# Optimization experiments

Hardware: AMD Instinct MI355X
Metric: run time of the kernel (lower is better)

## Reference

```python
import jax, jax.numpy as jnp
import numpy as np

PATCH = (4, 4, 4)
EMBED_DIM = 768
MASK_RATIO = 0.75
LN_EPS = 1e-3  # keras LayerNormalization default epsilon


def _sin_pos_enc_3d(nH, nW, nD, embed_dim):
    # Mirrors SinPosEncoding3D: per-axis sin/cos interleaved, concat, truncate.
    channels = int(np.ceil(embed_dim / 6) * 2)
    if channels % 2:
        channels += 1
    inv_freq = jnp.asarray(
        1.0 / np.power(10000, np.arange(0, channels, 2) / np.float32(channels)),
        dtype=jnp.float32)

    def emb1(n):
        s = jnp.arange(n, dtype=jnp.float32)[:, None] * inv_freq[None, :]  # [n, channels//2]
        return jnp.stack([jnp.sin(s), jnp.cos(s)], axis=-1).reshape(n, channels)

    ex = jnp.broadcast_to(emb1(nH)[:, None, None, :], (nH, nW, nD, channels))
    ey = jnp.broadcast_to(emb1(nW)[None, :, None, :], (nH, nW, nD, channels))
    ez = jnp.broadcast_to(emb1(nD)[None, None, :, :], (nH, nW, nD, channels))
    emb = jnp.concatenate([ex, ey, ez], axis=-1)[..., :embed_dim]
    return emb.reshape(1, nH * nW * nD, embed_dim)  # [1, token_num, E]


def setup_inputs() -> dict:
    key = jax.random.key(0)
    k1, k2, k3, k4 = jax.random.split(key, 4)
    B, H, W, D, C = 4, 96, 96, 96, 1
    nH, nW, nD = H // PATCH[0], W // PATCH[1], D // PATCH[2]
    token_num = nH * nW * nD
    mask_num = int(token_num * MASK_RATIO)
    patch_dim = PATCH[0] * PATCH[1] * PATCH[2] * C
    return {
        "x": jax.random.normal(k1, (B, H, W, D, C), dtype=jnp.float32),
        "proj_w": jax.random.normal(k2, (patch_dim, EMBED_DIM), dtype=jnp.float32) * 0.02,
        "proj_b": jnp.zeros((EMBED_DIM,), dtype=jnp.float32),
        "mask_token": jax.random.normal(k3, (1, mask_num, patch_dim), dtype=jnp.float32),
        "gamma": jnp.ones((EMBED_DIM,), dtype=jnp.float32),
        "beta": jnp.zeros((EMBED_DIM,), dtype=jnp.float32),
        "perm": jax.random.permutation(k4, token_num).astype(jnp.int32),
    }


def reference(x, proj_w, proj_b, mask_token, gamma, beta, perm):
    B, H, W, D, C = x.shape
    p0, p1, p2 = PATCH
    nH, nW, nD = H // p0, W // p1, D // p2
    token_num = nH * nW * nD
    mask_num = int(token_num * MASK_RATIO)

    # im2col-style 3D patch extraction (matches tf.extract_volume_patches layout)
    patches = x.reshape(B, nH, p0, nW, p1, nD, p2, C)
    patches = patches.transpose(0, 1, 3, 5, 2, 4, 6, 7)
    patches_flat = patches.reshape(B, token_num, p0 * p1 * p2 * C)

    mask_idx = perm[:mask_num]
    unmask_idx = perm[mask_num:]

    penc = _sin_pos_enc_3d(nH, nW, nD, EMBED_DIM)  # [1, token_num, E]

    # unmasked tokens: gather -> dense proj -> pos-enc add
    unmask_tokens = jnp.take(patches_flat, unmask_idx, axis=1)       # [B, U, pdim]
    a = jnp.einsum('bup,pe->bue', unmask_tokens, proj_w) + proj_b \
        + jnp.take(penc, unmask_idx, axis=1)                          # [B, U, E]

    # masked tokens: learned mask token -> proj -> pos-enc add, broadcast over B
    b = jnp.einsum('omp,pe->ome', mask_token, proj_w) + proj_b \
        + jnp.take(penc, mask_idx, axis=1)                            # [1, M, E]
    b = jnp.broadcast_to(b, (B, mask_num, EMBED_DIM))

    out = jnp.concatenate([a, b], axis=1).reshape(B, nH, nW, nD, EMBED_DIM)

    # LayerNorm over last axis (keras default: eps=1e-3)
    mean = jnp.mean(out, axis=-1, keepdims=True)
    var = jnp.var(out, axis=-1, keepdims=True)
    out = (out - mean) * jax.lax.rsqrt(var + LN_EPS) * gamma + beta
    return out, mask_idx
```

## Files before the change

kernel.cpp:

```cpp
#include <hip/hip_runtime.h>
#include <math.h>

#define NTHREADS 256
#define TROWS 16
#define TOKN 13824
#define MASKN 10368
#define UNMASKN 3456
#define EMB 768
#define NPOS 24
#define NBATCH 4
#define ABLOCKS (TOKN / TROWS)
#define BBLOCKS (MASKN / TROWS)
#define TABN (NPOS * 256)
#define WN (64 * EMB)

typedef __attribute__((ext_vector_type(8))) short short8;
typedef __attribute__((ext_vector_type(4))) float f32x4;

__device__ __forceinline__ short f2bf(float f) {
  union { float f; unsigned u; } c; c.f = f;
  unsigned u = c.u + 0x7FFFu + ((c.u >> 16) & 1u);
  return (short)(u >> 16);
}

__global__ __launch_bounds__(NTHREADS) void setup_kernel(
    const float* __restrict__ W, const int* __restrict__ perm,
    float* __restrict__ tabg, short* __restrict__ wsW,
    float* __restrict__ out_idx)
{
  int i = blockIdx.x * NTHREADS + threadIdx.x;
  if (i < MASKN) out_idx[i] = (float)perm[i];
  if (i < TABN) {
    const float c0 = 13.287712379549449f / 128.0f;
    int pos = i >> 8, e = i & 255, j = e >> 1;
    float s = (float)pos * exp2f(-(float)j * c0);
    tabg[i] = (e & 1) ? cosf(s) : sinf(s);
  }
  if (i < WN) {
    int col = i >> 6, k = i & 63;
    wsW[i] = f2bf(W[k * EMB + col]);
  }
}

__global__ __launch_bounds__(NTHREADS, 4) void fused_embed_ln_mfma(
    const float* __restrict__ x, const float* __restrict__ pb,
    const float* __restrict__ mt, const float* __restrict__ gmm,
    const float* __restrict__ bta, const int* __restrict__ perm,
    const float* __restrict__ tabg, const short* __restrict__ wsW,
    float* __restrict__ out)
{
  __shared__ __align__(16) short aLds[TROWS][72];
  __shared__ int segbase[3][TROWS];
  __shared__ float wred[TROWS][4][2];

  const int tid = threadIdx.x;
  const int blk = blockIdx.x;
  const bool isA = blk < ABLOCKS;

  {
    int t = tid >> 4, seg = tid & 15;
    int r;
    if (isA) {
      r = perm[MASKN + (blk * TROWS) % UNMASKN + t];
    } else {
      r = perm[(blk - ABLOCKS) * TROWS + t];
    }
    int h = r / 576; int rem = r - h * 576;
    int w = rem / 24; int d = rem - w * 24;
    if (seg < 3) segbase[seg][t] = (seg == 0 ? h : (seg == 1 ? w : d)) << 8;

    float4 v;
    if (isA) {
      int b = (blk * TROWS) / UNMASKN;
      int ph = seg >> 2, pw = seg & 3;
      v = *(const float4*)(x +
          ((((long)b * 96 + h * 4 + ph) * 96 + (w * 4 + pw)) * 96 + d * 4));
    } else {
      int m0 = (blk - ABLOCKS) * TROWS;
      v = *(const float4*)(mt + (long)(m0 + t) * 64 + seg * 4);
    }
    short4 s4; s4.x = f2bf(v.x); s4.y = f2bf(v.y); s4.z = f2bf(v.z); s4.w = f2bf(v.w);
    *(short4*)&aLds[t][seg * 4] = s4;
  }
  __syncthreads();

  const int wv = tid >> 6, lane = tid & 63;
  const int n16 = lane & 15, q = lane >> 4;
  const int q4 = q * 4;
  const int colbase = wv * 192;

  short8 af0 = *(const short8*)&aLds[n16][q * 8];
  short8 af1 = *(const short8*)&aLds[n16][32 + q * 8];

  f32x4 acc[12];
  const short* wp = wsW + (colbase + n16) * 64 + q * 8;
  #pragma unroll
  for (int jt = 0; jt < 12; ++jt) {
    short8 bf0 = *(const short8*)(wp + jt * 16 * 64);
    short8 bf1 = *(const short8*)(wp + jt * 16 * 64 + 32);
    f32x4 c = {0.f, 0.f, 0.f, 0.f};
    c = __builtin_amdgcn_mfma_f32_16x16x32_bf16(bf0, af0, c, 0, 0, 0);
    c = __builtin_amdgcn_mfma_f32_16x16x32_bf16(bf1, af1, c, 0, 0, 0);
    acc[jt] = c;
  }

  const float* t0 = tabg + segbase[0][n16];
  const float* t1 = tabg + segbase[1][n16];
  const float* t2 = tabg + segbase[2][n16];

  float s = 0.f, qq = 0.f;
  #pragma unroll
  for (int jt = 0; jt < 12; ++jt) {
    int colb = colbase + jt * 16 + q4;
    int seg = colb >> 8;
    int cb = colb & 255;
    const float* tp = (seg == 0) ? t0 : ((seg == 1) ? t1 : t2);
    f32x4 pbv = *(const f32x4*)(pb + colb);
    f32x4 tv  = *(const f32x4*)(tp + cb);
    float v0 = acc[jt][0] + pbv[0] + tv[0];
    float v1 = acc[jt][1] + pbv[1] + tv[1];
    float v2 = acc[jt][2] + pbv[2] + tv[2];
    float v3 = acc[jt][3] + pbv[3] + tv[3];
    acc[jt][0] = v0; acc[jt][1] = v1; acc[jt][2] = v2; acc[jt][3] = v3;
    s  += (v0 + v1) + (v2 + v3);
    qq += (v0 * v0 + v1 * v1) + (v2 * v2 + v3 * v3);
  }
  s  += __shfl_xor(s,  16, 64);
  s  += __shfl_xor(s,  32, 64);
  qq += __shfl_xor(qq, 16, 64);
  qq += __shfl_xor(qq, 32, 64);
  if (lane < 16) { wred[lane][wv][0] = s; wred[lane][wv][1] = qq; }
  __syncthreads();

  float ss = wred[n16][0][0] + wred[n16][1][0] + wred[n16][2][0] + wred[n16][3][0];
  float qs = wred[n16][0][1] + wred[n16][1][1] + wred[n16][2][1] + wred[n16][3][1];
  float mean = ss * (1.0f / 768.0f);
  float var = qs * (1.0f / 768.0f) - mean * mean;
  float rstd = 1.0f / sqrtf(var + 0.001f);

  if (isA) {
    int row0 = blk * TROWS;
    int b = row0 / UNMASKN;
    int u0 = row0 % UNMASKN;
    float* base = out + ((long)b * TOKN + u0 + n16) * EMB + colbase + q4;
    #pragma unroll
    for (int jt = 0; jt < 12; ++jt) {
      int colb = colbase + jt * 16 + q4;
      f32x4 g  = *(const f32x4*)(gmm + colb);
      f32x4 bb = *(const f32x4*)(bta + colb);
      f32x4 o;
      #pragma unroll
      for (int r = 0; r < 4; ++r) {
        float sc = rstd * g[r];
        o[r] = acc[jt][r] * sc + (bb[r] - mean * sc);
      }
      *(f32x4*)(base + jt * 16) = o;
    }
  } else {
    int m0 = (blk - ABLOCKS) * TROWS;
    float* base = out + ((long)UNMASKN + m0 + n16) * EMB + colbase + q4;
    #pragma unroll
    for (int jt = 0; jt < 12; ++jt) {
      int colb = colbase + jt * 16 + q4;
      f32x4 g  = *(const f32x4*)(gmm + colb);
      f32x4 bb = *(const f32x4*)(bta + colb);
      f32x4 o;
      #pragma unroll
      for (int r = 0; r < 4; ++r) {
        float sc = rstd * g[r];
        o[r] = acc[jt][r] * sc + (bb[r] - mean * sc);
      }
      float* p = base + jt * 16;
      #pragma unroll
      for (int b4 = 0; b4 < NBATCH; ++b4) {
        *(f32x4*)p = o;
        p += (long)TOKN * EMB;
      }
    }
  }
}

extern "C" void kernel_launch(void* const* d_in, const int* in_sizes, int n_in,
                              void* d_out, int out_size, void* d_ws, size_t ws_size,
                              hipStream_t stream) {
  const float* x    = (const float*)d_in[0];
  const float* W    = (const float*)d_in[1];
  const float* pb   = (const float*)d_in[2];
  const float* mt   = (const float*)d_in[3];
  const float* gmm  = (const float*)d_in[4];
  const float* bta  = (const float*)d_in[5];
  const int*   perm = (const int*)d_in[6];
  float* out = (float*)d_out;
  float* out_idx = out + (long)NBATCH * TOKN * EMB;

  float* tabg = (float*)d_ws;
  short* wsW  = (short*)((char*)d_ws + TABN * 4);

  setup_kernel<<<(WN + NTHREADS - 1) / NTHREADS, NTHREADS, 0, stream>>>(
      W, perm, tabg, wsW, out_idx);
  fused_embed_ln_mfma<<<ABLOCKS + BBLOCKS, NTHREADS, 0, stream>>>(
      x, pb, mt, gmm, bta, perm, tabg, wsW, out);
}
```

Baseline: 220.7 us.

## Stage LayerNorm output through LDS for coalesced stores; replicate mask blocks per batch

```diff
diff --git a/kernel.cpp b/kernel.cpp
--- a/kernel.cpp
+++ b/kernel.cpp
@@ -11,8 +11,10 @@
 #define NBATCH 4
 #define ABLOCKS (TOKN / TROWS)
 #define BBLOCKS (MASKN / TROWS)
+#define TOTBLOCKS (ABLOCKS + NBATCH * BBLOCKS)
 #define TABN (NPOS * 256)
 #define WN (64 * EMB)
+#define LROW 388
 
 typedef __attribute__((ext_vector_type(8))) short short8;
 typedef __attribute__((ext_vector_type(4))) float f32x4;
@@ -49,6 +51,7 @@
     const float* __restrict__ tabg, const short* __restrict__ wsW,
     float* __restrict__ out)
 {
+  __shared__ __align__(16) float ldsOut[TROWS * LROW];
   __shared__ __align__(16) short aLds[TROWS][72];
   __shared__ int segbase[3][TROWS];
   __shared__ float wred[TROWS][4][2];
@@ -56,6 +59,9 @@
   const int tid = threadIdx.x;
   const int blk = blockIdx.x;
   const bool isA = blk < ABLOCKS;
+  const int blkb = blk - ABLOCKS;
+  const int copy = isA ? 0 : (blkb / BBLOCKS);
+  const int bidx = isA ? 0 : (blkb % BBLOCKS);
 
   {
     int t = tid >> 4, seg = tid & 15;
@@ -63,7 +69,7 @@
     if (isA) {
       r = perm[MASKN + (blk * TROWS) % UNMASKN + t];
     } else {
-      r = perm[(blk - ABLOCKS) * TROWS + t];
+      r = perm[bidx * TROWS + t];
     }
     int h = r / 576; int rem = r - h * 576;
     int w = rem / 24; int d = rem - w * 24;
@@ -76,8 +82,7 @@
       v = *(const float4*)(x +
           ((((long)b * 96 + h * 4 + ph) * 96 + (w * 4 + pw)) * 96 + d * 4));
     } else {
-      int m0 = (blk - ABLOCKS) * TROWS;
-      v = *(const float4*)(mt + (long)(m0 + t) * 64 + seg * 4);
+      v = *(const float4*)(mt + (long)(bidx * TROWS + t) * 64 + seg * 4);
     }
     short4 s4; s4.x = f2bf(v.x); s4.y = f2bf(v.y); s4.z = f2bf(v.z); s4.w = f2bf(v.w);
     *(short4*)&aLds[t][seg * 4] = s4;
@@ -138,45 +143,43 @@
   float var = qs * (1.0f / 768.0f) - mean * mean;
   float rstd = 1.0f / sqrtf(var + 0.001f);
 
+  long rowbase;
   if (isA) {
     int row0 = blk * TROWS;
-    int b = row0 / UNMASKN;
-    int u0 = row0 % UNMASKN;
-    float* base = out + ((long)b * TOKN + u0 + n16) * EMB + colbase + q4;
+    rowbase = (long)(row0 / UNMASKN) * TOKN + (row0 % UNMASKN);
+  } else {
+    rowbase = (long)copy * TOKN + UNMASKN + bidx * TROWS;
+  }
+  float* gbase = out + rowbase * EMB;
+  const int mychunk = wv >> 1;
+
+  #pragma unroll
+  for (int c = 0; c < 2; ++c) {
+    if (mychunk == c) {
+      #pragma unroll
+      for (int jt = 0; jt < 12; ++jt) {
+        int colb = colbase + jt * 16 + q4;
+        f32x4 g  = *(const f32x4*)(gmm + colb);
+        f32x4 bb = *(const f32x4*)(bta + colb);
+        f32x4 o;
+        #pragma unroll
+        for (int r = 0; r < 4; ++r) {
+          float sc = rstd * g[r];
+          o[r] = acc[jt][r] * sc + (bb[r] - mean * sc);
+        }
+        *(f32x4*)&ldsOut[n16 * LROW + (colb - c * 384)] = o;
+      }
+    }
+    __syncthreads();
     #pragma unroll
-    for (int jt = 0; jt < 12; ++jt) {
-      int colb = colbase + jt * 16 + q4;
-      f32x4 g  = *(const f32x4*)(gmm + colb);
-      f32x4 bb = *(const f32x4*)(bta + colb);
-      f32x4 o;
-      #pragma unroll
-      for (int r = 0; r < 4; ++r) {
-        float sc = rstd * g[r];
-        o[r] = acc[jt][r] * sc + (bb[r] - mean * sc);
-      }
-      *(f32x4*)(base + jt * 16) = o;
-    }
-  } else {
-    int m0 = (blk - ABLOCKS) * TROWS;
-    float* base = out + ((long)UNMASKN + m0 + n16) * EMB + colbase + q4;
-    #pragma unroll
-    for (int jt = 0; jt < 12; ++jt) {
-      int colb = colbase + jt * 16 + q4;
-      f32x4 g  = *(const f32x4*)(gmm + colb);
-      f32x4 bb = *(const f32x4*)(bta + colb);
-      f32x4 o;
-      #pragma unroll
-      for (int r = 0; r < 4; ++r) {
-        float sc = rstd * g[r];
-        o[r] = acc[jt][r] * sc + (bb[r] - mean * sc);
-      }
-      float* p = base + jt * 16;
-      #pragma unroll
-      for (int b4 = 0; b4 < NBATCH; ++b4) {
-        *(f32x4*)p = o;
-        p += (long)TOKN * EMB;
-      }
-    }
+    for (int p = 0; p < 6; ++p) {
+      int idx = p * 256 + tid;
+      int row = idx / 96;
+      int off = idx - row * 96;
+      f32x4 v = *(const f32x4*)&ldsOut[row * LROW + off * 4];
+      *(f32x4*)(gbase + (long)row * EMB + c * 384 + off * 4) = v;
+    }
+    if (c == 0) __syncthreads();
   }
 }
 
@@ -198,6 +201,6 @@
 
   setup_kernel<<<(WN + NTHREADS - 1) / NTHREADS, NTHREADS, 0, stream>>>(
       W, perm, tabg, wsW, out_idx);
-  fused_embed_ln_mfma<<<ABLOCKS + BBLOCKS, NTHREADS, 0, stream>>>(
+  fused_embed_ln_mfma<<<TOTBLOCKS, NTHREADS, 0, stream>>>(
       x, pb, mt, gmm, bta, perm, tabg, wsW, out);
 }
```

New measurement: 254.8 us. +15.4%, slower.

## Process 32 tokens per block and keep weight fragments in registers

Applied to the files above, without the earlier changes.

```diff
diff --git a/kernel.cpp b/kernel.cpp
--- a/kernel.cpp
+++ b/kernel.cpp
@@ -2,15 +2,17 @@
 #include <math.h>
 
 #define NTHREADS 256
-#define TROWS 16
+#define TPB 32
 #define TOKN 13824
 #define MASKN 10368
 #define UNMASKN 3456
 #define EMB 768
 #define NPOS 24
 #define NBATCH 4
-#define ABLOCKS (TOKN / TROWS)
-#define BBLOCKS (MASKN / TROWS)
+#define APB (UNMASKN / TPB)
+#define ABLK (NBATCH * APB)
+#define BBLK (MASKN / TPB)
+#define TOTBLK (ABLK + BBLK)
 #define TABN (NPOS * 256)
 #define WN (64 * EMB)
 
@@ -42,141 +44,146 @@
   }
 }
 
-__global__ __launch_bounds__(NTHREADS, 4) void fused_embed_ln_mfma(
+__global__ __launch_bounds__(NTHREADS) void fused_embed_ln_mfma(
     const float* __restrict__ x, const float* __restrict__ pb,
     const float* __restrict__ mt, const float* __restrict__ gmm,
     const float* __restrict__ bta, const int* __restrict__ perm,
     const float* __restrict__ tabg, const short* __restrict__ wsW,
     float* __restrict__ out)
 {
-  __shared__ __align__(16) short aLds[TROWS][72];
-  __shared__ int segbase[3][TROWS];
-  __shared__ float wred[TROWS][4][2];
+  __shared__ __align__(16) short aLds[TPB][72];
+  __shared__ int segb[3][TPB];
+  __shared__ float wred[16][4][2];
 
   const int tid = threadIdx.x;
   const int blk = blockIdx.x;
-  const bool isA = blk < ABLOCKS;
-
-  {
-    int t = tid >> 4, seg = tid & 15;
-    int r;
-    if (isA) {
-      r = perm[MASKN + (blk * TROWS) % UNMASKN + t];
-    } else {
-      r = perm[(blk - ABLOCKS) * TROWS + t];
-    }
+  const bool isA = blk < ABLK;
+  const int b  = isA ? (blk / APB) : 0;
+  const int u0 = isA ? ((blk % APB) * TPB) : 0;
+  const int m0 = isA ? 0 : ((blk - ABLK) * TPB);
+
+  #pragma unroll
+  for (int half = 0; half < 2; ++half) {
+    int task = half * 256 + tid;
+    int t = task >> 4, seg = task & 15;
+    int r = isA ? perm[MASKN + u0 + t] : perm[m0 + t];
     int h = r / 576; int rem = r - h * 576;
     int w = rem / 24; int d = rem - w * 24;
-    if (seg < 3) segbase[seg][t] = (seg == 0 ? h : (seg == 1 ? w : d)) << 8;
+    if (seg < 3) segb[seg][t] = (seg == 0 ? h : (seg == 1 ? w : d)) << 8;
 
     float4 v;
     if (isA) {
-      int b = (blk * TROWS) / UNMASKN;
       int ph = seg >> 2, pw = seg & 3;
       v = *(const float4*)(x +
           ((((long)b * 96 + h * 4 + ph) * 96 + (w * 4 + pw)) * 96 + d * 4));
     } else {
-      int m0 = (blk - ABLOCKS) * TROWS;
       v = *(const float4*)(mt + (long)(m0 + t) * 64 + seg * 4);
     }
     short4 s4; s4.x = f2bf(v.x); s4.y = f2bf(v.y); s4.z = f2bf(v.z); s4.w = f2bf(v.w);
     *(short4*)&aLds[t][seg * 4] = s4;
   }
-  __syncthreads();
 
   const int wv = tid >> 6, lane = tid & 63;
   const int n16 = lane & 15, q = lane >> 4;
   const int q4 = q * 4;
   const int colbase = wv * 192;
 
-  short8 af0 = *(const short8*)&aLds[n16][q * 8];
-  short8 af1 = *(const short8*)&aLds[n16][32 + q * 8];
-
-  f32x4 acc[12];
-  const short* wp = wsW + (colbase + n16) * 64 + q * 8;
+  short8 wf0[12], wf1[12];
+  {
+    const short* wp = wsW + (colbase + n16) * 64 + q * 8;
+    #pragma unroll
+    for (int jt = 0; jt < 12; ++jt) {
+      wf0[jt] = *(const short8*)(wp + jt * 1024);
+      wf1[jt] = *(const short8*)(wp + jt * 1024 + 32);
+    }
+  }
+  __syncthreads();
+
   #pragma unroll
-  for (int jt = 0; jt < 12; ++jt) {
-    short8 bf0 = *(const short8*)(wp + jt * 16 * 64);
-    short8 bf1 = *(const short8*)(wp + jt * 16 * 64 + 32);
-    f32x4 c = {0.f, 0.f, 0.f, 0.f};
-    c = __builtin_amdgcn_mfma_f32_16x16x32_bf16(bf0, af0, c, 0, 0, 0);
-    c = __builtin_amdgcn_mfma_f32_16x16x32_bf16(bf1, af1, c, 0, 0, 0);
-    acc[jt] = c;
-  }
-
-  const float* t0 = tabg + segbase[0][n16];
-  const float* t1 = tabg + segbase[1][n16];
-  const float* t2 = tabg + segbase[2][n16];
-
-  float s = 0.f, qq = 0.f;
-  #pragma unroll
-  for (int jt = 0; jt < 12; ++jt) {
-    int colb = colbase + jt * 16 + q4;
-    int seg = colb >> 8;
-    int cb = colb & 255;
-    const float* tp = (seg == 0) ? t0 : ((seg == 1) ? t1 : t2);
-    f32x4 pbv = *(const f32x4*)(pb + colb);
-    f32x4 tv  = *(const f32x4*)(tp + cb);
-    float v0 = acc[jt][0] + pbv[0] + tv[0];
-    float v1 = acc[jt][1] + pbv[1] + tv[1];
-    float v2 = acc[jt][2] + pbv[2] + tv[2];
-    float v3 = acc[jt][3] + pbv[3] + tv[3];
-    acc[jt][0] = v0; acc[jt][1] = v1; acc[jt][2] = v2; acc[jt][3] = v3;
-    s  += (v0 + v1) + (v2 + v3);
-    qq += (v0 * v0 + v1 * v1) + (v2 * v2 + v3 * v3);
-  }
-  s  += __shfl_xor(s,  16, 64);
-  s  += __shfl_xor(s,  32, 64);
-  qq += __shfl_xor(qq, 16, 64);
-  qq += __shfl_xor(qq, 32, 64);
-  if (lane < 16) { wred[lane][wv][0] = s; wred[lane][wv][1] = qq; }
-  __syncthreads();
-
-  float ss = wred[n16][0][0] + wred[n16][1][0] + wred[n16][2][0] + wred[n16][3][0];
-  float qs = wred[n16][0][1] + wred[n16][1][1] + wred[n16][2][1] + wred[n16][3][1];
-  float mean = ss * (1.0f / 768.0f);
-  float var = qs * (1.0f / 768.0f) - mean * mean;
-  float rstd = 1.0f / sqrtf(var + 0.001f);
-
-  if (isA) {
-    int row0 = blk * TROWS;
-    int b = row0 / UNMASKN;
-    int u0 = row0 % UNMASKN;
-    float* base = out + ((long)b * TOKN + u0 + n16) * EMB + colbase + q4;
+  for (int g = 0; g < 2; ++g) {
+    const int trow = g * 16 + n16;
+    short8 af0 = *(const short8*)&aLds[trow][q * 8];
+    short8 af1 = *(const short8*)&aLds[trow][32 + q * 8];
+
+    f32x4 acc[12];
+    #pragma unroll
+    for (int jt = 0; jt < 12; ++jt) {
+      f32x4 c = {0.f, 0.f, 0.f, 0.f};
+      c = __builtin_amdgcn_mfma_f32_16x16x32_bf16(wf0[jt], af0, c, 0, 0, 0);
+      c = __builtin_amdgcn_mfma_f32_16x16x32_bf16(wf1[jt], af1, c, 0, 0, 0);
+      acc[jt] = c;
+    }
+
+    const float* t0 = tabg + segb[0][trow];
+    const float* t1 = tabg + segb[1][trow];
+    const float* t2 = tabg + segb[2][trow];
+    float s = 0.f, qq = 0.f;
     #pragma unroll
     for (int jt = 0; jt < 12; ++jt) {
       int colb = colbase + jt * 16 + q4;
-      f32x4 g  = *(const f32x4*)(gmm + colb);
-      f32x4 bb = *(const f32x4*)(bta + colb);
-      f32x4 o;
+      int seg = colb >> 8;
+      int cb = colb & 255;
+      const float* tp = (seg == 0) ? t0 : ((seg == 1) ? t1 : t2);
+      f32x4 pbv = *(const f32x4*)(pb + colb);
+      f32x4 tv  = *(const f32x4*)(tp + cb);
+      float v0 = acc[jt][0] + pbv[0] + tv[0];
+      float v1 = acc[jt][1] + pbv[1] + tv[1];
+      float v2 = acc[jt][2] + pbv[2] + tv[2];
+      float v3 = acc[jt][3] + pbv[3] + tv[3];
+      acc[jt][0] = v0; acc[jt][1] = v1; acc[jt][2] = v2; acc[jt][3] = v3;
+      s  += (v0 + v1) + (v2 + v3);
+      qq += (v0 * v0 + v1 * v1) + (v2 * v2 + v3 * v3);
+    }
+    s  += __shfl_xor(s,  16, 64);
+    s  += __shfl_xor(s,  32, 64);
+    qq += __shfl_xor(qq, 16, 64);
+    qq += __shfl_xor(qq, 32, 64);
+    if (lane < 16) { wred[lane][wv][0] = s; wred[lane][wv][1] = qq; }
+    __syncthreads();
+
+    float ss = wred[n16][0][0] + wred[n16][1][0] + wred[n16][2][0] + wred[n16][3][0];
+    float qs = wred[n16][0][1] + wred[n16][1][1] + wred[n16][2][1] + wred[n16][3][1];
+    float mean = ss * (1.0f / 768.0f);
+    float var = qs * (1.0f / 768.0f) - mean * mean;
+    float rstd = 1.0f / sqrtf(var + 0.001f);
+
+    if (isA) {
+      float* base = out + ((long)b * TOKN + u0 + trow) * EMB + colbase + q4;
       #pragma unroll
-      for (int r = 0; r < 4; ++r) {
-        float sc = rstd * g[r];
-        o[r] = acc[jt][r] * sc + (bb[r] - mean * sc);
+      for (int jt = 0; jt < 12; ++jt) {
+        int colb = colbase + jt * 16 + q4;
+        f32x4 gg = *(const f32x4*)(gmm + colb);
+        f32x4 bb = *(const f32x4*)(bta + colb);
+        f32x4 o;
+        #pragma unroll
+        for (int r = 0; r < 4; ++r) {
+          float sc = rstd * gg[r];
+          o[r] = acc[jt][r] * sc + (bb[r] - mean * sc);
+        }
+        *(f32x4*)(base + jt * 16) = o;
       }
-      *(f32x4*)(base + jt * 16) = o;
-    }
-  } else {
-    int m0 = (blk - ABLOCKS) * TROWS;
-    float* base = out + ((long)UNMASKN + m0 + n16) * EMB + colbase + q4;
-    #pragma unroll
-    for (int jt = 0; jt < 12; ++jt) {
-      int colb = colbase + jt * 16 + q4;
-      f32x4 g  = *(const f32x4*)(gmm + colb);
-      f32x4 bb = *(const f32x4*)(bta + colb);
-      f32x4 o;
+    } else {
+      float* base = out + ((long)UNMASKN + m0 + trow) * EMB + colbase + q4;
       #pragma unroll
-      for (int r = 0; r < 4; ++r) {
-        float sc = rstd * g[r];
-        o[r] = acc[jt][r] * sc + (bb[r] - mean * sc);
+      for (int jt = 0; jt < 12; ++jt) {
+        int colb = colbase + jt * 16 + q4;
+        f32x4 gg = *(const f32x4*)(gmm + colb);
+        f32x4 bb = *(const f32x4*)(bta + colb);
+        f32x4 o;
+        #pragma unroll
+        for (int r = 0; r < 4; ++r) {
+          float sc = rstd * gg[r];
+          o[r] = acc[jt][r] * sc + (bb[r] - mean * sc);
+        }
+        float* p = base + jt * 16;
+        #pragma unroll
+        for (int b4 = 0; b4 < NBATCH; ++b4) {
+          *(f32x4*)p = o;
+          p += (long)TOKN * EMB;
+        }
       }
-      float* p = base + jt * 16;
-      #pragma unroll
-      for (int b4 = 0; b4 < NBATCH; ++b4) {
-        *(f32x4*)p = o;
-        p += (long)TOKN * EMB;
-      }
-    }
+    }
+    if (g == 0) __syncthreads();
   }
 }
 
@@ -198,6 +205,6 @@
 
   setup_kernel<<<(WN + NTHREADS - 1) / NTHREADS, NTHREADS, 0, stream>>>(
       W, perm, tabg, wsW, out_idx);
-  fused_embed_ln_mfma<<<ABLOCKS + BBLOCKS, NTHREADS, 0, stream>>>(
+  fused_embed_ln_mfma<<<TOTBLK, NTHREADS, 0, stream>>>(
       x, pb, mt, gmm, bta, perm, tabg, wsW, out);
 }
```

Result: faster. 215.6 us (-2.3%).
